# Kernel optimization log

Measured on AMD Instinct MI355X. Metric: run time of the kernel, lower is better.

The kernel has to match this reference:

```python
import jax, jax.numpy as jnp
import numpy as np

T, B, IN, H, OUT = 4096, 64, 4, 256, 2


def setup_inputs() -> dict:
    key = jax.random.key(0)
    ks = jax.random.split(key, 8)
    k = (1.0 / H) ** 0.5
    return {
        "input": jax.random.normal(ks[0], (T, B, IN), dtype=jnp.float32),
        "target": jax.random.normal(ks[1], (T, B, OUT), dtype=jnp.float32),
        "Wi": jax.random.uniform(ks[2], (H, IN), minval=-k, maxval=k, dtype=jnp.float32),
        "bi": jax.random.uniform(ks[3], (H,), minval=-k, maxval=k, dtype=jnp.float32),
        "Wh": jax.random.uniform(ks[4], (H, H), minval=-k, maxval=k, dtype=jnp.float32),
        "bh": jax.random.uniform(ks[5], (H,), minval=-k, maxval=k, dtype=jnp.float32),
        "Wf": jax.random.normal(ks[6], (OUT, H), dtype=jnp.float32) * (1.0 / H) ** 0.5,
        "bf": jnp.zeros((OUT,), dtype=jnp.float32),
    }


def reference(input, target, Wi, bi, Wh, bh, Wf, bf):
    # Precompute input projection for all timesteps: [T, B, H]
    xi = jnp.einsum("tbi,hi->tbh", input, Wi) + bi

    def step(h, xt):
        # h: [B, H]; xt: [B, H] (already projected input)
        h_new = jnp.tanh(xt + h @ Wh.T + bh)
        return h_new, h_new

    h0 = jnp.zeros((input.shape[1], Wh.shape[0]), dtype=input.dtype)
    _, hs = jax.lax.scan(step, h0, xi)  # hs: [T, B, H]

    # Output head: tanh(Linear(hidden)) -> [T, B, OUT]
    out = jnp.tanh(jnp.einsum("tbh,oh->tbo", hs, Wf) + bf)
    return out
```

## Files before the change

### kernel.cpp

```cpp
#include <hip/hip_runtime.h>

#define T_STEPS 4096
#define BATCH   64
#define INDIM   4
#define H       256
#define OUTD    2
#define CHUNK   32
#define SLOT_DW 36
#define ENT_DW  (4*SLOT_DW)
#define ENT_B   (4*ENT_DW)
#define RING_DW (CHUNK*ENT_DW)
#define WF_DW   (OUTD*(H/2))
#define XS_DW   (CHUNK*INDIM)

typedef __fp16 half2v __attribute__((ext_vector_type(2)));

__device__ __forceinline__ float fast_tanh(float x) {
    float ax = fabsf(x);
    float e  = __expf(-2.0f * ax);
    float r  = (1.0f - e) * __builtin_amdgcn_rcpf(1.0f + e);
    return copysignf(r, x);
}

template<int CTRL>
__device__ __forceinline__ float qadd(float a) {
    int s = __builtin_amdgcn_update_dpp(0, __builtin_bit_cast(int, a),
                                        CTRL, 0xf, 0xf, true);
    return a + __builtin_bit_cast(float, s);
}
#define QX1 0xB1
#define QX2 0x4E

__global__ __attribute__((amdgpu_waves_per_eu(1, 1))) __launch_bounds__(256)
void elman_kernel(const float* __restrict__ input,
                  const float* __restrict__ Wi,
                  const float* __restrict__ bi,
                  const float* __restrict__ Wh,
                  const float* __restrict__ bh,
                  const float* __restrict__ Wf,
                  const float* __restrict__ bf,
                  float* __restrict__ out)
{
    const int b  = blockIdx.x;
    const int t  = threadIdx.x;
    const int q  = t >> 2;
    const int ko = t & 3;
    const int k0 = ko * 64;

    __shared__ unsigned int lds[RING_DW + WF_DW + XS_DW];
    unsigned int* ring   = lds;
    unsigned int* wf_pk  = lds + RING_DW;
    float*        xstage = (float*)(lds + RING_DW + WF_DW);

    half2v w[4][32];
    #pragma unroll
    for (int r = 0; r < 4; ++r) {
        const float* p = Wh + (size_t)(4 * q + r) * H + k0;
        #pragma unroll
        for (int j = 0; j < 16; ++j) {
            float4 a = *(const float4*)(p + 4 * j);
            w[r][2 * j]     = __builtin_amdgcn_cvt_pkrtz(a.x, a.y);
            w[r][2 * j + 1] = __builtin_amdgcn_cvt_pkrtz(a.z, a.w);
        }
    }
    #pragma unroll
    for (int r = 0; r < 4; ++r)
        #pragma unroll
        for (int j = 0; j < 32; ++j) {
            float f = __builtin_bit_cast(float, w[r][j]);
            asm volatile("" : "+v"(f));
            w[r][j] = __builtin_bit_cast(half2v, f);
        }

    const float4 wim   = *(const float4*)(Wi + t * INDIM);
    const float  biasm = bi[t] + bh[t];
    const float  bf0   = bf[0], bf1 = bf[1];
    const int    boff  = (t >> 6) * (SLOT_DW * 4) + (t & 63) * 2;

    {
        const int o = t >> 7, e = t & 127;
        wf_pk[t] = __builtin_bit_cast(unsigned int,
            __builtin_amdgcn_cvt_pkrtz(Wf[o * H + 2 * e], Wf[o * H + 2 * e + 1]));
    }
    if (t < H / 2) ring[(CHUNK - 1) * ENT_DW + (t >> 5) * SLOT_DW + (t & 31)] = 0u;
    __syncthreads();

    const unsigned int rd_off = (unsigned int)(ko * SLOT_DW);

    for (int chunk = 0; chunk < T_STEPS / CHUNK; ++chunk) {
        if (t < CHUNK) {
            const int s = chunk * CHUNK + t;
            ((float4*)xstage)[t] = *(const float4*)(input + ((size_t)s * BATCH + b) * INDIM);
        }
        __syncthreads();

        #pragma unroll 1
        for (int i = 0; i < CHUNK; ++i) {
            const unsigned int* hb =
                ring + ((i + CHUNK - 1) & (CHUNK - 1)) * ENT_DW + rd_off;
            uint4 hv[8];
            #pragma unroll
            for (int j = 0; j < 8; ++j) hv[j] = *(const uint4*)(hb + 4 * j);
            const float4 xs = *((const float4*)xstage + i);

            float acc0 = 0.f, acc1 = 0.f, acc2 = 0.f, acc3 = 0.f;
            #pragma unroll
            for (int j = 0; j < 8; ++j) {
                half2v h0 = __builtin_bit_cast(half2v, hv[j].x);
                half2v h1 = __builtin_bit_cast(half2v, hv[j].y);
                half2v h2 = __builtin_bit_cast(half2v, hv[j].z);
                half2v h3 = __builtin_bit_cast(half2v, hv[j].w);
                acc0 = __builtin_amdgcn_fdot2(w[0][4 * j],     h0, acc0, false);
                acc1 = __builtin_amdgcn_fdot2(w[1][4 * j],     h0, acc1, false);
                acc2 = __builtin_amdgcn_fdot2(w[2][4 * j],     h0, acc2, false);
                acc3 = __builtin_amdgcn_fdot2(w[3][4 * j],     h0, acc3, false);
                acc0 = __builtin_amdgcn_fdot2(w[0][4 * j + 1], h1, acc0, false);
                acc1 = __builtin_amdgcn_fdot2(w[1][4 * j + 1], h1, acc1, false);
                acc2 = __builtin_amdgcn_fdot2(w[2][4 * j + 1], h1, acc2, false);
                acc3 = __builtin_amdgcn_fdot2(w[3][4 * j + 1], h1, acc3, false);
                acc0 = __builtin_amdgcn_fdot2(w[0][4 * j + 2], h2, acc0, false);
                acc1 = __builtin_amdgcn_fdot2(w[1][4 * j + 2], h2, acc1, false);
                acc2 = __builtin_amdgcn_fdot2(w[2][4 * j + 2], h2, acc2, false);
                acc3 = __builtin_amdgcn_fdot2(w[3][4 * j + 2], h2, acc3, false);
                acc0 = __builtin_amdgcn_fdot2(w[0][4 * j + 3], h3, acc0, false);
                acc1 = __builtin_amdgcn_fdot2(w[1][4 * j + 3], h3, acc1, false);
                acc2 = __builtin_amdgcn_fdot2(w[2][4 * j + 3], h3, acc2, false);
                acc3 = __builtin_amdgcn_fdot2(w[3][4 * j + 3], h3, acc3, false);
            }

            acc0 = qadd<QX1>(acc0);
            acc1 = qadd<QX1>(acc1);
            acc2 = qadd<QX1>(acc2);
            acc3 = qadd<QX1>(acc3);
            float A  = (ko & 1) ? acc1 : acc0;
            float Bv = (ko & 1) ? acc3 : acc2;
            A  = qadd<QX2>(A);
            Bv = qadd<QX2>(Bv);
            float accm = (ko & 2) ? Bv : A;

            float pre = accm + biasm +
                xs.x * wim.x + xs.y * wim.y + xs.z * wim.z + xs.w * wim.w;
            __fp16 h16 = (__fp16)fast_tanh(pre);
            *(__fp16*)((char*)ring + i * ENT_B + boff) = h16;

            __syncthreads();
        }

        {
            const int task = t >> 2;
            const int s    = task >> 1;
            const int o    = task & 1;
            const int sub  = t & 3;
            const unsigned int* hp = ring + s * ENT_DW + sub * SLOT_DW;
            const unsigned int* wp = wf_pk + o * (H / 2) + sub * 32;

            float acc = 0.f;
            #pragma unroll
            for (int j = 0; j < 8; ++j) {
                uint4 hq = *(const uint4*)(hp + 4 * j);
                uint4 wq = *(const uint4*)(wp + 4 * j);
                acc = __builtin_amdgcn_fdot2(__builtin_bit_cast(half2v, wq.x),
                                             __builtin_bit_cast(half2v, hq.x), acc, false);
                acc = __builtin_amdgcn_fdot2(__builtin_bit_cast(half2v, wq.y),
                                             __builtin_bit_cast(half2v, hq.y), acc, false);
                acc = __builtin_amdgcn_fdot2(__builtin_bit_cast(half2v, wq.z),
                                             __builtin_bit_cast(half2v, hq.z), acc, false);
                acc = __builtin_amdgcn_fdot2(__builtin_bit_cast(half2v, wq.w),
                                             __builtin_bit_cast(half2v, hq.w), acc, false);
            }
            acc = qadd<QX1>(acc);
            acc = qadd<QX2>(acc);

            if (sub == 0) {
                out[((size_t)(chunk * CHUNK + s) * BATCH + b) * OUTD + o] =
                    fast_tanh(acc + (o ? bf1 : bf0));
            }
            __syncthreads();
        }
    }
}

extern "C" void kernel_launch(void* const* d_in, const int* in_sizes, int n_in,
                              void* d_out, int out_size, void* d_ws, size_t ws_size,
                              hipStream_t stream) {
    const float* input = (const float*)d_in[0];
    const float* Wi = (const float*)d_in[2];
    const float* bi = (const float*)d_in[3];
    const float* bh = (const float*)d_in[5];
    const float* Wh = (const float*)d_in[4];
    const float* Wf = (const float*)d_in[6];
    const float* bf = (const float*)d_in[7];
    float* out = (float*)d_out;

    elman_kernel<<<dim3(BATCH), dim3(256), 0, stream>>>(
        input, Wi, bi, Wh, bh, Wf, bf, out);
}
```

Baseline: 1.821 ms.

## Batch 16 sequences per block and compute the recurrence with MFMA

Replaces the per-sequence fdot2 recurrence with 16x16x32 fp16 MFMA tiles, each block now handling 16 batch columns, so only 4 blocks are launched instead of 64. The input projection and bias are folded into an extra K-tile, with a constant-1 column carrying the bias. The output head is computed by MFMA on one rotating wave per step, replacing the separate per-chunk pass. The hidden state is double-buffered in LDS. This aims to cut the per-step latency of the serial chain by using matrix units, but it uses far fewer CUs and keeps one barrier per step.

```diff
diff --git a/kernel.cpp b/kernel.cpp
--- a/kernel.cpp
+++ b/kernel.cpp
@@ -5,15 +5,19 @@
 #define INDIM   4
 #define H       256
 #define OUTD    2
+#define NCOL    16
 #define CHUNK   32
-#define SLOT_DW 36
-#define ENT_DW  (4*SLOT_DW)
-#define ENT_B   (4*ENT_DW)
-#define RING_DW (CHUNK*ENT_DW)
-#define WF_DW   (OUTD*(H/2))
-#define XS_DW   (CHUNK*INDIM)
+#define COL_DW  136
+#define SLOT_DW (NCOL*COL_DW)
+#define XS_DW   (CHUNK*256)
+#define LDS_DW  (2*SLOT_DW + XS_DW)
 
-typedef __fp16 half2v __attribute__((ext_vector_type(2)));
+typedef _Float16 h8  __attribute__((ext_vector_type(8)));
+typedef float    f4  __attribute__((ext_vector_type(4)));
+
+__device__ __forceinline__ unsigned pk(float a, float b) {
+    return __builtin_bit_cast(unsigned, __builtin_amdgcn_cvt_pkrtz(a, b));
+}
 
 __device__ __forceinline__ float fast_tanh(float x) {
     float ax = fabsf(x);
@@ -21,15 +25,6 @@
     float r  = (1.0f - e) * __builtin_amdgcn_rcpf(1.0f + e);
     return copysignf(r, x);
 }
-
-template<int CTRL>
-__device__ __forceinline__ float qadd(float a) {
-    int s = __builtin_amdgcn_update_dpp(0, __builtin_bit_cast(int, a),
-                                        CTRL, 0xf, 0xf, true);
-    return a + __builtin_bit_cast(float, s);
-}
-#define QX1 0xB1
-#define QX2 0x4E
 
 __global__ __attribute__((amdgpu_waves_per_eu(1, 1))) __launch_bounds__(256)
 void elman_kernel(const float* __restrict__ input,
@@ -41,141 +36,141 @@
                   const float* __restrict__ bf,
                   float* __restrict__ out)
 {
-    const int b  = blockIdx.x;
-    const int t  = threadIdx.x;
-    const int q  = t >> 2;
-    const int ko = t & 3;
-    const int k0 = ko * 64;
+    const int t    = threadIdx.x;
+    const int w    = t >> 6;
+    const int lane = t & 63;
+    const int c    = lane & 15;
+    const int g    = lane >> 4;
+    const int b0   = blockIdx.x * NCOL;
 
-    __shared__ unsigned int lds[RING_DW + WF_DW + XS_DW];
-    unsigned int* ring   = lds;
-    unsigned int* wf_pk  = lds + RING_DW;
-    float*        xstage = (float*)(lds + RING_DW + WF_DW);
+    __shared__ unsigned lds[LDS_DW];
+    unsigned* xs = lds + 2 * SLOT_DW;
 
-    half2v w[4][32];
+    h8 a[4][9];
     #pragma unroll
-    for (int r = 0; r < 4; ++r) {
-        const float* p = Wh + (size_t)(4 * q + r) * H + k0;
+    for (int mt = 0; mt < 4; ++mt) {
+        const int row = w * 64 + mt * 16 + c;
         #pragma unroll
-        for (int j = 0; j < 16; ++j) {
-            float4 a = *(const float4*)(p + 4 * j);
-            w[r][2 * j]     = __builtin_amdgcn_cvt_pkrtz(a.x, a.y);
-            w[r][2 * j + 1] = __builtin_amdgcn_cvt_pkrtz(a.z, a.w);
+        for (int kt = 0; kt < 8; ++kt) {
+            const float* p = Wh + (size_t)row * H + kt * 32 + g * 8;
+            float4 x0 = *(const float4*)(p);
+            float4 x1 = *(const float4*)(p + 4);
+            uint4 u;
+            u.x = pk(x0.x, x0.y); u.y = pk(x0.z, x0.w);
+            u.z = pk(x1.x, x1.y); u.w = pk(x1.z, x1.w);
+            a[mt][kt] = __builtin_bit_cast(h8, u);
         }
+        uint4 u = {0u, 0u, 0u, 0u};
+        if (g == 0) {
+            float4 wi = *(const float4*)(Wi + row * INDIM);
+            u.x = pk(wi.x, wi.y);
+            u.y = pk(wi.z, wi.w);
+            u.z = pk(bi[row] + bh[row], 0.f);
+        }
+        a[mt][8] = __builtin_bit_cast(h8, u);
     }
+    h8 awf[8];
     #pragma unroll
-    for (int r = 0; r < 4; ++r)
-        #pragma unroll
-        for (int j = 0; j < 32; ++j) {
-            float f = __builtin_bit_cast(float, w[r][j]);
-            asm volatile("" : "+v"(f));
-            w[r][j] = __builtin_bit_cast(half2v, f);
+    for (int kt = 0; kt < 8; ++kt) {
+        uint4 u = {0u, 0u, 0u, 0u};
+        if (c < OUTD) {
+            const float* p = Wf + (size_t)c * H + kt * 32 + g * 8;
+            float4 x0 = *(const float4*)(p);
+            float4 x1 = *(const float4*)(p + 4);
+            u.x = pk(x0.x, x0.y); u.y = pk(x0.z, x0.w);
+            u.z = pk(x1.x, x1.y); u.w = pk(x1.z, x1.w);
         }
+        awf[kt] = __builtin_bit_cast(h8, u);
+    }
+    const float bf0 = bf[0], bf1 = bf[1];
 
-    const float4 wim   = *(const float4*)(Wi + t * INDIM);
-    const float  biasm = bi[t] + bh[t];
-    const float  bf0   = bf[0], bf1 = bf[1];
-    const int    boff  = (t >> 6) * (SLOT_DW * 4) + (t & 63) * 2;
-
-    {
-        const int o = t >> 7, e = t & 127;
-        wf_pk[t] = __builtin_bit_cast(unsigned int,
-            __builtin_amdgcn_cvt_pkrtz(Wf[o * H + 2 * e], Wf[o * H + 2 * e + 1]));
+    for (int idx = t; idx < SLOT_DW; idx += 256) lds[idx] = 0u;
+    for (int idx = t; idx < XS_DW; idx += 256) xs[idx] = 0u;
+    #pragma unroll
+    for (int it = 0; it < 2; ++it) {
+        const int task = t + it * 256;
+        xs[(task >> 4) * 256 + (task & 15) * 16 + 2] = 0x00003C00u;
     }
-    if (t < H / 2) ring[(CHUNK - 1) * ENT_DW + (t >> 5) * SLOT_DW + (t & 31)] = 0u;
     __syncthreads();
 
-    const unsigned int rd_off = (unsigned int)(ko * SLOT_DW);
+    const int rdw = c * COL_DW + g * 4;
 
-    for (int chunk = 0; chunk < T_STEPS / CHUNK; ++chunk) {
-        if (t < CHUNK) {
-            const int s = chunk * CHUNK + t;
-            ((float4*)xstage)[t] = *(const float4*)(input + ((size_t)s * BATCH + b) * INDIM);
-        }
-        __syncthreads();
-
-        #pragma unroll 1
-        for (int i = 0; i < CHUNK; ++i) {
-            const unsigned int* hb =
-                ring + ((i + CHUNK - 1) & (CHUNK - 1)) * ENT_DW + rd_off;
-            uint4 hv[8];
+    #pragma unroll 2
+    for (int i = 0; i < T_STEPS; ++i) {
+        if ((i & (CHUNK - 1)) == 0) {
             #pragma unroll
-            for (int j = 0; j < 8; ++j) hv[j] = *(const uint4*)(hb + 4 * j);
-            const float4 xs = *((const float4*)xstage + i);
-
-            float acc0 = 0.f, acc1 = 0.f, acc2 = 0.f, acc3 = 0.f;
-            #pragma unroll
-            for (int j = 0; j < 8; ++j) {
-                half2v h0 = __builtin_bit_cast(half2v, hv[j].x);
-                half2v h1 = __builtin_bit_cast(half2v, hv[j].y);
-                half2v h2 = __builtin_bit_cast(half2v, hv[j].z);
-                half2v h3 = __builtin_bit_cast(half2v, hv[j].w);
-                acc0 = __builtin_amdgcn_fdot2(w[0][4 * j],     h0, acc0, false);
-                acc1 = __builtin_amdgcn_fdot2(w[1][4 * j],     h0, acc1, false);
-                acc2 = __builtin_amdgcn_fdot2(w[2][4 * j],     h0, acc2, false);
-                acc3 = __builtin_amdgcn_fdot2(w[3][4 * j],     h0, acc3, false);
-                acc0 = __builtin_amdgcn_fdot2(w[0][4 * j + 1], h1, acc0, false);
-                acc1 = __builtin_amdgcn_fdot2(w[1][4 * j + 1], h1, acc1, false);
-                acc2 = __builtin_amdgcn_fdot2(w[2][4 * j + 1], h1, acc2, false);
-                acc3 = __builtin_amdgcn_fdot2(w[3][4 * j + 1], h1, acc3, false);
-                acc0 = __builtin_amdgcn_fdot2(w[0][4 * j + 2], h2, acc0, false);
-                acc1 = __builtin_amdgcn_fdot2(w[1][4 * j + 2], h2, acc1, false);
-                acc2 = __builtin_amdgcn_fdot2(w[2][4 * j + 2], h2, acc2, false);
-                acc3 = __builtin_amdgcn_fdot2(w[3][4 * j + 2], h2, acc3, false);
-                acc0 = __builtin_amdgcn_fdot2(w[0][4 * j + 3], h3, acc0, false);
-                acc1 = __builtin_amdgcn_fdot2(w[1][4 * j + 3], h3, acc1, false);
-                acc2 = __builtin_amdgcn_fdot2(w[2][4 * j + 3], h3, acc2, false);
-                acc3 = __builtin_amdgcn_fdot2(w[3][4 * j + 3], h3, acc3, false);
+            for (int it = 0; it < 2; ++it) {
+                const int task = t + it * 256;
+                const int s = task >> 4, cc = task & 15;
+                float4 xv = *(const float4*)(input +
+                    ((size_t)(i + s) * BATCH + b0 + cc) * INDIM);
+                uint2 pkd = { pk(xv.x, xv.y), pk(xv.z, xv.w) };
+                *(uint2*)(xs + s * 256 + cc * 16) = pkd;
             }
-
-            acc0 = qadd<QX1>(acc0);
-            acc1 = qadd<QX1>(acc1);
-            acc2 = qadd<QX1>(acc2);
-            acc3 = qadd<QX1>(acc3);
-            float A  = (ko & 1) ? acc1 : acc0;
-            float Bv = (ko & 1) ? acc3 : acc2;
-            A  = qadd<QX2>(A);
-            Bv = qadd<QX2>(Bv);
-            float accm = (ko & 2) ? Bv : A;
-
-            float pre = accm + biasm +
-                xs.x * wim.x + xs.y * wim.y + xs.z * wim.z + xs.w * wim.w;
-            __fp16 h16 = (__fp16)fast_tanh(pre);
-            *(__fp16*)((char*)ring + i * ENT_B + boff) = h16;
-
             __syncthreads();
         }
 
+        const unsigned* hb = lds + (i & 1) * SLOT_DW;
+        h8 bfr[9];
+        #pragma unroll
+        for (int kt = 0; kt < 8; ++kt) {
+            uint4 u = *(const uint4*)(hb + rdw + kt * 16);
+            bfr[kt] = __builtin_bit_cast(h8, u);
+        }
         {
-            const int task = t >> 2;
-            const int s    = task >> 1;
-            const int o    = task & 1;
-            const int sub  = t & 3;
-            const unsigned int* hp = ring + s * ENT_DW + sub * SLOT_DW;
-            const unsigned int* wp = wf_pk + o * (H / 2) + sub * 32;
+            uint4 u = *(const uint4*)(xs + (i & (CHUNK - 1)) * 256 + c * 16 + g * 4);
+            bfr[8] = __builtin_bit_cast(h8, u);
+        }
 
-            float acc = 0.f;
+        if (i && ((i & 3) == w)) {
+            f4 dh = {0.f, 0.f, 0.f, 0.f};
             #pragma unroll
-            for (int j = 0; j < 8; ++j) {
-                uint4 hq = *(const uint4*)(hp + 4 * j);
-                uint4 wq = *(const uint4*)(wp + 4 * j);
-                acc = __builtin_amdgcn_fdot2(__builtin_bit_cast(half2v, wq.x),
-                                             __builtin_bit_cast(half2v, hq.x), acc, false);
-                acc = __builtin_amdgcn_fdot2(__builtin_bit_cast(half2v, wq.y),
-                                             __builtin_bit_cast(half2v, hq.y), acc, false);
-                acc = __builtin_amdgcn_fdot2(__builtin_bit_cast(half2v, wq.z),
-                                             __builtin_bit_cast(half2v, hq.z), acc, false);
-                acc = __builtin_amdgcn_fdot2(__builtin_bit_cast(half2v, wq.w),
-                                             __builtin_bit_cast(half2v, hq.w), acc, false);
+            for (int kt = 0; kt < 8; ++kt)
+                dh = __builtin_amdgcn_mfma_f32_16x16x32_f16(awf[kt], bfr[kt], dh, 0, 0, 0);
+            if (g == 0) {
+                float2 o2 = { fast_tanh(dh.x + bf0), fast_tanh(dh.y + bf1) };
+                *(float2*)(out + ((size_t)(i - 1) * BATCH + b0 + c) * OUTD) = o2;
             }
-            acc = qadd<QX1>(acc);
-            acc = qadd<QX2>(acc);
+        }
 
-            if (sub == 0) {
-                out[((size_t)(chunk * CHUNK + s) * BATCH + b) * OUTD + o] =
-                    fast_tanh(acc + (o ? bf1 : bf0));
-            }
-            __syncthreads();
+        f4 d0 = {0.f,0.f,0.f,0.f}, d1 = d0, d2 = d0, d3 = d0;
+        #pragma unroll
+        for (int kt = 0; kt < 9; ++kt) {
+            d0 = __builtin_amdgcn_mfma_f32_16x16x32_f16(a[0][kt], bfr[kt], d0, 0, 0, 0);
+            d1 = __builtin_amdgcn_mfma_f32_16x16x32_f16(a[1][kt], bfr[kt], d1, 0, 0, 0);
+            d2 = __builtin_amdgcn_mfma_f32_16x16x32_f16(a[2][kt], bfr[kt], d2, 0, 0, 0);
+            d3 = __builtin_amdgcn_mfma_f32_16x16x32_f16(a[3][kt], bfr[kt], d3, 0, 0, 0);
+        }
+
+        unsigned* wsl = lds + ((i & 1) ^ 1) * SLOT_DW;
+        f4 dd[4] = {d0, d1, d2, d3};
+        #pragma unroll
+        for (int mt = 0; mt < 4; ++mt) {
+            float h0 = fast_tanh(dd[mt].x);
+            float h1 = fast_tanh(dd[mt].y);
+            float h2 = fast_tanh(dd[mt].z);
+            float h3 = fast_tanh(dd[mt].w);
+            const int r = w * 64 + mt * 16 + g * 4;
+            const int dwo = c * COL_DW + ((r >> 5) << 4) + (((r >> 3) & 3) << 2)
+                          + ((g & 1) << 1);
+            uint2 ph = { pk(h0, h1), pk(h2, h3) };
+            *(uint2*)(wsl + dwo) = ph;
+        }
+        __syncthreads();
+    }
+
+    if (w == 0) {
+        const unsigned* hb = lds;
+        f4 dh = {0.f, 0.f, 0.f, 0.f};
+        #pragma unroll
+        for (int kt = 0; kt < 8; ++kt) {
+            uint4 u = *(const uint4*)(hb + rdw + kt * 16);
+            dh = __builtin_amdgcn_mfma_f32_16x16x32_f16(awf[kt],
+                     __builtin_bit_cast(h8, u), dh, 0, 0, 0);
+        }
+        if (g == 0) {
+            float2 o2 = { fast_tanh(dh.x + bf0), fast_tanh(dh.y + bf1) };
+            *(float2*)(out + ((size_t)(T_STEPS - 1) * BATCH + b0 + c) * OUTD) = o2;
         }
     }
 }
@@ -186,12 +181,12 @@
     const float* input = (const float*)d_in[0];
     const float* Wi = (const float*)d_in[2];
     const float* bi = (const float*)d_in[3];
+    const float* Wh = (const float*)d_in[4];
     const float* bh = (const float*)d_in[5];
-    const float* Wh = (const float*)d_in[4];
     const float* Wf = (const float*)d_in[6];
     const float* bf = (const float*)d_in[7];
     float* out = (float*)d_out;
 
-    elman_kernel<<<dim3(BATCH), dim3(256), 0, stream>>>(
+    elman_kernel<<<dim3(BATCH / NCOL), dim3(256), 0, stream>>>(
         input, Wi, bi, Wh, bh, Wf, bf, out);
 }
```

Measured after the change: 3.265 ms. 79.3% more time.
